# Performance work log

Hardware: AMD Instinct MI355X
Metric: run time of the kernel (lower is better)

Reference implementation:

```python
import jax, jax.numpy as jnp
import numpy as np

B, S, C, T = 256, 128, 64, 60
ENC, COL, RNN, ATT, ACT, TYP = 512, 512, 512, 512, 128, 64
NPROD, NTYPE = 97, 32
LS, PTEMP, CTEMP = 0.2, 1.0, 1.0
NEG = -1e9


def setup_inputs() -> dict:
    key = jax.random.key(0)
    ks = jax.random.split(key, 24)
    enc = jax.random.normal(ks[0], (B, S, ENC), jnp.float32)
    col_enc = jax.random.normal(ks[1], (B, C, COL), jnp.float32)
    enc_lens = jax.random.randint(ks[2], (B,), 1, S + 1)
    col_lens = jax.random.randint(ks[3], (B,), 1, C + 1)
    action_kind = jax.random.randint(ks[4], (B, T), 0, 3)  # 0=ApplyRule,1=Reduce,2=SelectColumn
    tgt_lens = jax.random.randint(ks[5], (B,), 1, T + 1)
    prod_ids = jax.random.randint(ks[6], (B, T), 0, NPROD)
    col_ids = jax.random.randint(ks[7], (B, T), 0, C) % col_lens[:, None]
    parent_prod = jax.random.randint(ks[8], (B, T), 0, NPROD)
    parent_type = jax.random.randint(ks[9], (B, T), 0, NTYPE)
    parent_time = jax.random.randint(ks[10], (B, T), 0, T) % jnp.maximum(jnp.arange(T), 1)[None, :]
    g = lambda k, shp: jax.random.normal(k, shp, jnp.float32) * 0.02
    IN = ACT + ATT + ACT + TYP + RNN  # a_tm1 | att_tm1 | parent_prod | parent_type | parent_h
    return dict(
        enc=enc, col_enc=col_enc, enc_lens=enc_lens, col_lens=col_lens,
        action_kind=action_kind, tgt_lens=tgt_lens, prod_ids=prod_ids,
        col_ids=col_ids, parent_prod=parent_prod, parent_type=parent_type,
        parent_time=parent_time,
        prod_embed=g(ks[11], (NPROD + 1, ACT)),
        type_embed=g(ks[12], (NTYPE, TYP)),
        b_lin=jnp.zeros((NPROD + 1,), jnp.float32),
        W_ih=g(ks[13], (IN, 4 * RNN)), W_hh=g(ks[14], (RNN, 4 * RNN)),
        b_lstm=jnp.zeros((4 * RNN,), jnp.float32),
        W_att_q=g(ks[15], (RNN, ENC)),
        W_att_vec=g(ks[16], (ENC + RNN, ATT)),
        W_r1=g(ks[17], (ATT, 4 * ATT)), b_r1=jnp.zeros((4 * ATT,), jnp.float32),
        W_r2=g(ks[18], (4 * ATT, ACT)), b_r2=jnp.zeros((ACT,), jnp.float32),
        W_col_in=g(ks[19], (COL, ACT)),
        W_ptr=g(ks[20], (ATT, COL)),
        w_mem=g(ks[21], (ATT, 1)),
    )


def reference(enc, col_enc, enc_lens, col_lens, action_kind, tgt_lens, prod_ids,
              col_ids, parent_prod, parent_type, parent_time,
              prod_embed, type_embed, b_lin, W_ih, W_hh, b_lstm,
              W_att_q, W_att_vec, W_r1, b_r1, W_r2, b_r2,
              W_col_in, W_ptr, w_mem):
    enc_mask = jnp.arange(S)[None, :] < enc_lens[:, None]   # [B,S]
    col_valid = jnp.arange(C)[None, :] < col_lens[:, None]  # [B,C]
    col_in_embed = jnp.einsum('bcd,da->bca', col_enc, W_col_in)  # column_rnn_input, [B,C,ACT]

    # previous-step actions (a_{t-1}); dummy zeros at t=0 (x is zeroed there anyway)
    shift = lambda a: jnp.concatenate([jnp.zeros_like(a[:, :1]), a[:, :-1]], axis=1)
    kind_p, pid_p, cid_p = shift(action_kind), shift(prod_ids), shift(col_ids)

    def scan_step(carry, xs):
        h, c, att, hist, appear, acc = carry
        t, kp, pp, cp, kind, pid, cid, fprod, ftype, ptime = xs
        # --- prep step input ---
        prev_valid = (t - 1) < tgt_lens
        e_rule = prod_embed[jnp.where(kp == 1, NPROD, pp)]                      # [B,ACT]
        e_col = jnp.take_along_axis(col_in_embed, cp[:, None, None], axis=1)[:, 0]
        a_embed = jnp.where((kp == 2)[:, None], e_col, e_rule)
        a_embed = jnp.where(prev_valid[:, None], a_embed, 0.0)
        parent_h = hist[ptime, jnp.arange(B)]                                   # [B,RNN]
        x = jnp.concatenate([a_embed, att, prod_embed[fprod], type_embed[ftype], parent_h], axis=-1)
        x = jnp.where(t == 0, 0.0, x)
        # --- LSTMCell (torch gate order i,f,g,o) ---
        gates = x @ W_ih + h @ W_hh + b_lstm
        i, f, g_, o = jnp.split(gates, 4, axis=-1)
        c_new = jax.nn.sigmoid(f) * c + jax.nn.sigmoid(i) * jnp.tanh(g_)
        h_new = jax.nn.sigmoid(o) * jnp.tanh(c_new)
        # --- attention over encoder ---
        scores = jnp.einsum('bd,bsd->bs', h_new @ W_att_q, enc)
        scores = jnp.where(enc_mask, scores, NEG)
        ctx = jnp.einsum('bs,bsd->bd', jax.nn.softmax(scores, axis=-1), enc)
        att_new = jnp.tanh(jnp.concatenate([ctx, h_new], axis=-1) @ W_att_vec)
        # --- production readout (tied output embedding) ---
        emb_q = jnp.tanh(att_new @ W_r1 + b_r1) @ W_r2 + b_r2
        rule_lp = jax.nn.log_softmax((emb_q @ prod_embed.T + b_lin) / PTEMP, axis=-1)
        # --- pointer net over columns with memory gate ---
        gate = jax.nn.sigmoid(att_new @ w_mem)                                  # [B,1]
        w_c = jnp.einsum('bd,bcd->bc', att_new @ W_ptr, col_enc)
        weights = w_c * appear * gate + w_c * (1.0 - appear) * (1.0 - gate)
        weights = jnp.where(col_valid, weights, NEG) / CTEMP
        col_lp = jax.nn.log_softmax(weights, axis=-1)
        # --- per-example log prob of gold action ---
        valid = t < tgt_lens
        lp_rule = jnp.take_along_axis(rule_lp, jnp.where(kind == 1, NPROD, pid)[:, None], axis=1)[:, 0]
        lp_col_raw = jnp.take_along_axis(col_lp, cid[:, None], axis=1)[:, 0]
        col_sum = jnp.sum(jnp.where(col_valid, col_lp, 0.0), axis=-1)
        lp_col = (1.0 - LS) * lp_col_raw + LS * col_sum / col_lens
        lp = jnp.where(kind == 2, lp_col, lp_rule)
        acc = acc + jnp.where(valid, lp, 0.0)
        # --- state updates (appear mask updated after use, matching torch) ---
        appear = jnp.maximum(appear, ((kind == 2) & valid)[:, None] * jax.nn.one_hot(cid, C, dtype=appear.dtype))
        hist = hist.at[t].set(h_new)
        return (h_new, c_new, att_new, hist, appear, acc), None

    carry0 = (
        jnp.zeros((B, RNN), jnp.float32), jnp.zeros((B, RNN), jnp.float32),
        jnp.zeros((B, ATT), jnp.float32), jnp.zeros((T, B, RNN), jnp.float32),
        jnp.zeros((B, C), jnp.float32), jnp.zeros((B,), jnp.float32),
    )
    xs = (jnp.arange(T), kind_p.T, pid_p.T, cid_p.T, action_kind.T, prod_ids.T,
          col_ids.T, parent_prod.T, parent_type.T, parent_time.T)
    (_, _, _, _, _, acc), _ = jax.lax.scan(scan_step, carry0, xs)
    return -jnp.mean(acc)
```

## Files before the change

### kernel.cpp

```cpp
#include <hip/hip_runtime.h>
#include <math.h>

#define NB 256
#define NS 128
#define NCOL 64
#define NT 60
#define DENC 512
#define DRNN 512
#define DATT 512
#define DACT 128
#define DTYP 64
#define DG 2048
#define NEGV (-1e9f)
#define NBH 131072
#define NROW 15360
#define RPW 512
#define NRP 2624

typedef unsigned short ushort_t;
typedef __attribute__((ext_vector_type(8))) short short8;
typedef __attribute__((ext_vector_type(4))) float f32x4;

__device__ __forceinline__ float sigf(float x) { return 1.0f / (1.0f + __expf(-x)); }
__device__ __forceinline__ float tanhfast(float x) {
  x = fminf(fmaxf(x, -15.0f), 15.0f);
  float e = __expf(-2.0f * x);
  return (1.0f - e) / (1.0f + e);
}
__device__ __forceinline__ ushort_t f2bf(float f) {
  union { float f; unsigned u; } v; v.f = f;
  unsigned r = v.u + 0x7fffu + ((v.u >> 16) & 1u);
  return (ushort_t)(r >> 16);
}
__device__ __forceinline__ float bf2f(ushort_t b) {
  union { unsigned u; float f; } v; v.u = ((unsigned)b) << 16; return v.f;
}
__device__ __forceinline__ short8 cvt8(const float* p) {
  f32x4 x = *(const f32x4*)p, y = *(const f32x4*)(p + 4);
  short8 r;
  r[0]=(short)f2bf(x[0]); r[1]=(short)f2bf(x[1]); r[2]=(short)f2bf(x[2]); r[3]=(short)f2bf(x[3]);
  r[4]=(short)f2bf(y[0]); r[5]=(short)f2bf(y[1]); r[6]=(short)f2bf(y[2]); r[7]=(short)f2bf(y[3]);
  return r;
}

__global__ __launch_bounds__(256) void zero_kernel(float* __restrict__ p, int n) {
  int i = blockIdx.x * 256 + threadIdx.x;
  if (i < n) p[i] = 0.0f;
}

__global__ __launch_bounds__(256) void cvt_bf16_kernel(const float* __restrict__ src,
    ushort_t* __restrict__ dst, int n8)
{
  int i = blockIdx.x * 256 + threadIdx.x;
  if (i < n8) *(short8*)&dst[(size_t)i * 8] = cvt8(src + (size_t)i * 8);
}

__global__ __launch_bounds__(256) void pack_w(const float* __restrict__ src,
    ushort_t* __restrict__ dst, int Ksub, int Nsub, int Ntot, int K0, int N0, int ldsrc)
{
  int idx = blockIdx.x * 256 + threadIdx.x;
  if (idx >= Ksub * Nsub) return;
  int k = idx / Nsub, n = idx - k * Nsub;
  int gk = K0 + k;
  dst[((size_t)(gk >> 3) * Ntot + (N0 + n)) * 8 + (gk & 7)] =
      f2bf(src[(size_t)k * ldsrc + n]);
}

__global__ __launch_bounds__(256) void pack_wT(const float* __restrict__ W,
    ushort_t* __restrict__ dst)
{
  int idx = blockIdx.x * 256 + threadIdx.x;
  if (idx >= 512 * 512) return;
  int r = idx >> 9, d = idx & 511;
  dst[((size_t)(d >> 3) * 512 + r) * 8 + (d & 7)] = f2bf(W[(size_t)r * 512 + d]);
}

__global__ __launch_bounds__(256) void r2p_kernel(const float* __restrict__ W_r2,
    const float* __restrict__ prod_embed, const float* __restrict__ b_r2,
    const float* __restrict__ b_lin, ushort_t* __restrict__ Wr2p,
    float* __restrict__ bias2)
{
  int idx = blockIdx.x * 256 + threadIdx.x;
  if (idx >= 2049 * 98) return;
  int k = idx / 98, j = idx - k * 98;
  const float* pe = prod_embed + (size_t)j * DACT;
  if (k < 2048) {
    const float* wr = W_r2 + (size_t)k * DACT;
    float a = 0.f;
    #pragma unroll 8
    for (int d = 0; d < DACT; ++d) a = fmaf(wr[d], pe[d], a);
    Wr2p[((size_t)(k >> 3) * 128 + j) * 8 + (k & 7)] = f2bf(a);
  } else {
    float a = b_lin[j];
    #pragma unroll 8
    for (int d = 0; d < DACT; ++d) a = fmaf(b_r2[d], pe[d], a);
    bias2[j] = a;
  }
}

__global__ __launch_bounds__(64) void appear_kernel(const int* __restrict__ action_kind,
    const int* __restrict__ tgt_lens, const int* __restrict__ col_ids,
    float* __restrict__ appear_all)
{
  int b = blockIdx.x, c = threadIdx.x;
  float ap = 0.f;
  int tl = tgt_lens[b];
  for (int t = 0; t < NT; ++t) {
    appear_all[((size_t)t * NB + b) * 64 + c] = ap;
    if (t < tl && action_kind[b * NT + t] == 2 && col_ids[b * NT + t] == c) ap = 1.f;
  }
}

__global__ __launch_bounds__(256) void gemm_bf16(
    const float* __restrict__ A1, int lda1,
    const ushort_t* __restrict__ Bp, ushort_t* __restrict__ Cb, int ldc,
    int N, int K)
{
  __shared__ short As[2][4096];
  __shared__ short Bs[2][4096];
  const int tid = threadIdx.x;
  const int lane = tid & 63, w = tid >> 6;
  const int wr = w >> 1, wc = w & 1;
  const int mBase = blockIdx.y * 64, nBase = blockIdx.x * 64;
  const int nt = K >> 6;
  f32x4 ra0[2], ra1[2];
  short8 rb[2];
  auto issue = [&](int kt) {
    #pragma unroll
    for (int s = 0; s < 2; ++s) {
      int slot = tid + s * 256;
      int kc = slot >> 6, m = slot & 63;
      int k0 = (kt << 6) + kc * 8;
      const float* p = A1 + (size_t)(mBase + m) * lda1 + k0;
      ra0[s] = *(const f32x4*)p;
      ra1[s] = *(const f32x4*)(p + 4);
      rb[s] = *(const short8*)(Bp + ((size_t)(k0 >> 3) * N + nBase + m) * 8);
    }
  };
  auto store = [&](int buf) {
    #pragma unroll
    for (int s = 0; s < 2; ++s) {
      int slot = tid + s * 256;
      short8 av;
      av[0]=(short)f2bf(ra0[s][0]); av[1]=(short)f2bf(ra0[s][1]);
      av[2]=(short)f2bf(ra0[s][2]); av[3]=(short)f2bf(ra0[s][3]);
      av[4]=(short)f2bf(ra1[s][0]); av[5]=(short)f2bf(ra1[s][1]);
      av[6]=(short)f2bf(ra1[s][2]); av[7]=(short)f2bf(ra1[s][3]);
      *(short8*)&As[buf][slot * 8] = av;
      *(short8*)&Bs[buf][slot * 8] = rb[s];
    }
  };
  f32x4 z4 = {0.f,0.f,0.f,0.f};
  f32x4 acc[2][2] = {{z4,z4},{z4,z4}};
  issue(0); store(0);
  __syncthreads();
  int cur = 0;
  for (int kt = 0; kt < nt; ++kt) {
    bool more = (kt + 1 < nt);
    if (more) issue(kt + 1);
    #pragma unroll
    for (int kk = 0; kk < 2; ++kk) {
      int ko = kk * 4 + (lane >> 4);
      short8 af[2], bfr[2];
      #pragma unroll
      for (int f = 0; f < 2; ++f) {
        int row = wr * 32 + f * 16 + (lane & 15);
        af[f] = *(const short8*)&As[cur][(ko * 64 + row) * 8];
        int col = wc * 32 + f * 16 + (lane & 15);
        bfr[f] = *(const short8*)&Bs[cur][(ko * 64 + col) * 8];
      }
      #pragma unroll
      for (int i = 0; i < 2; ++i)
        #pragma unroll
        for (int j = 0; j < 2; ++j)
          acc[i][j] = __builtin_amdgcn_mfma_f32_16x16x32_bf16(af[i], bfr[j], acc[i][j], 0, 0, 0);
    }
    if (more) store(cur ^ 1);
    __syncthreads();
    cur ^= 1;
  }
  #pragma unroll
  for (int i = 0; i < 2; ++i)
    #pragma unroll
    for (int j = 0; j < 2; ++j)
      #pragma unroll
      for (int r = 0; r < 4; ++r) {
        int row = mBase + wr * 32 + i * 16 + (lane >> 4) * 4 + r;
        int col = nBase + wc * 32 + j * 16 + (lane & 15);
        Cb[(size_t)row * ldc + col] = f2bf(acc[i][j][r]);
      }
}

__global__ __launch_bounds__(256) void gemm_encwq(
    const float* __restrict__ enc, const ushort_t* __restrict__ WqTp,
    ushort_t* __restrict__ encWq, ushort_t* __restrict__ enc_b)
{
  __shared__ short Asm[32768];
  const int tid = threadIdx.x;
  const int lane = tid & 63, w = tid >> 6;
  const int wr = w >> 1, wc = w & 1;
  const int mBase = blockIdx.x * 64;
  #pragma unroll
  for (int it = 0; it < 16; ++it) {
    int o = tid + it * 256;
    int row = o >> 6, c = o & 63;
    short8 v = cvt8(enc + (size_t)(mBase + row) * 512 + c * 8);
    *(short8*)&Asm[row * 512 + ((c ^ (row & 7)) * 8)] = v;
    *(short8*)(enc_b + (size_t)(mBase + row) * 512 + c * 8) = v;
  }
  __syncthreads();
  for (int nt = 0; nt < 8; ++nt) {
    f32x4 z4 = {0.f,0.f,0.f,0.f};
    f32x4 acc[2][2] = {{z4,z4},{z4,z4}};
    short8 bb[2][4];
    auto loadBf = [&](int kt, short8* dst) {
      #pragma unroll
      for (int kk = 0; kk < 2; ++kk)
        #pragma unroll
        for (int f = 0; f < 2; ++f) {
          int ko = kt * 8 + kk * 4 + (lane >> 4);
          int col = nt * 64 + wc * 32 + f * 16 + (lane & 15);
          dst[kk * 2 + f] = *(const short8*)(WqTp + ((size_t)ko * 512 + col) * 8);
        }
    };
    loadBf(0, bb[0]);
    loadBf(1, bb[1]);
    #pragma unroll
    for (int kt = 0; kt < 8; ++kt) {
      short8 cur[4];
      #pragma unroll
      for (int i = 0; i < 4; ++i) cur[i] = bb[kt & 1][i];
      if (kt + 2 < 8) loadBf(kt + 2, bb[kt & 1]);
      #pragma unroll
      for (int kk = 0; kk < 2; ++kk) {
        int ko = kt * 8 + kk * 4 + (lane >> 4);
        short8 af[2];
        #pragma unroll
        for (int f = 0; f < 2; ++f) {
          int row = wr * 32 + f * 16 + (lane & 15);
          af[f] = *(const short8*)&Asm[row * 512 + ((ko ^ (row & 7)) * 8)];
        }
        #pragma unroll
        for (int i = 0; i < 2; ++i)
          #pragma unroll
          for (int j = 0; j < 2; ++j)
            acc[i][j] = __builtin_amdgcn_mfma_f32_16x16x32_bf16(af[i], cur[kk * 2 + j], acc[i][j], 0, 0, 0);
      }
    }
    #pragma unroll
    for (int i = 0; i < 2; ++i)
      #pragma unroll
      for (int j = 0; j < 2; ++j)
        #pragma unroll
        for (int r = 0; r < 4; ++r) {
          int row = mBase + wr * 32 + i * 16 + (lane >> 4) * 4 + r;
          int col = nt * 64 + wc * 32 + j * 16 + (lane & 15);
          encWq[(size_t)row * 512 + col] = f2bf(acc[i][j][r]);
        }
  }
}

template <class FA, class FB, class FE>
__device__ __forceinline__ void gemm_core(char* smem, FA loadA, FB loadB,
    int ktBeg, int ktEnd, FE epi)
{
  short* As = (short*)smem;
  short* Bs = (short*)smem + 8192;
  const int tid = threadIdx.x;
  const int lane = tid & 63, w = tid >> 6;
  const int wr = w >> 1, wc = w & 1;
  f32x4 z4 = {0.f,0.f,0.f,0.f};
  f32x4 acc[2][2] = {{z4,z4},{z4,z4}};
  short8 pa[2], pb[2];
  auto issue = [&](int kt) {
    #pragma unroll
    for (int s = 0; s < 2; ++s) {
      int slot = tid + s * 256;
      int kc = slot >> 6;
      int k = (kt << 6) + (kc << 3);
      pa[s] = loadA(k);
      pb[s] = loadB(slot & 63, k);
    }
  };
  auto store = [&](int buf) {
    #pragma unroll
    for (int s = 0; s < 2; ++s) {
      int slot = tid + s * 256;
      *(short8*)&As[buf * 4096 + slot * 8] = pa[s];
      *(short8*)&Bs[buf * 4096 + slot * 8] = pb[s];
    }
  };
  issue(ktBeg); store(0);
  __syncthreads();
  int cur = 0;
  for (int kt = ktBeg; kt < ktEnd; ++kt) {
    bool more = (kt + 1 < ktEnd);
    if (more) issue(kt + 1);
    #pragma unroll
    for (int kk = 0; kk < 2; ++kk) {
      int ko = kk * 4 + (lane >> 4);
      short8 af[2], bfr[2];
      #pragma unroll
      for (int f = 0; f < 2; ++f) {
        int row = wr * 32 + f * 16 + (lane & 15);
        af[f] = *(const short8*)&As[cur * 4096 + (ko * 64 + row) * 8];
        int col = wc * 32 + f * 16 + (lane & 15);
        bfr[f] = *(const short8*)&Bs[cur * 4096 + (ko * 64 + col) * 8];
      }
      #pragma unroll
      for (int i = 0; i < 2; ++i)
        #pragma unroll
        for (int j = 0; j < 2; ++j)
          acc[i][j] = __builtin_amdgcn_mfma_f32_16x16x32_bf16(af[i], bfr[j], acc[i][j], 0, 0, 0);
    }
    if (more) store(cur ^ 1);
    __syncthreads();
    cur ^= 1;
  }
  #pragma unroll
  for (int i = 0; i < 2; ++i)
    #pragma unroll
    for (int j = 0; j < 2; ++j)
      #pragma unroll
      for (int r = 0; r < 4; ++r) {
        int rl = wr * 32 + i * 16 + (lane >> 4) * 4 + r;
        int cl = wc * 32 + j * 16 + (lane & 15);
        epi(rl, cl, acc[i][j][r]);
      }
}

__global__ __launch_bounds__(256) void k1_gates(
    const int* __restrict__ action_kind, const int* __restrict__ tgt_lens,
    const int* __restrict__ prod_ids, const int* __restrict__ col_ids,
    const int* __restrict__ parent_prod, const int* __restrict__ parent_type,
    const int* __restrict__ parent_time,
    const float* __restrict__ prod_embed, const float* __restrict__ type_embed,
    const ushort_t* __restrict__ WpG, const ushort_t* __restrict__ colin_b,
    const ushort_t* __restrict__ att_all, const ushort_t* __restrict__ hist_u,
    float* __restrict__ gates0, float* __restrict__ gates1,
    float* __restrict__ gates2, float* __restrict__ gates3, int t)
{
  __shared__ __align__(16) char smem[32768];
  const int tid = threadIdx.x;
  const int nb = blockIdx.x, mb = blockIdx.y, ks = blockIdx.z;
  const int mBase = mb * 64, nBase = nb * 64;
  const int b = mBase + (tid & 63);
  int kp = action_kind[b * NT + t - 1];
  int pp = prod_ids[b * NT + t - 1];
  int cp = col_ids[b * NT + t - 1];
  bool pv = (t - 1) < tgt_lens[b];
  int fp = parent_prod[b * NT + t];
  int ft = parent_type[b * NT + t];
  int ptm = parent_time[b * NT + t];
  const ushort_t* hist_prev = hist_u + (size_t)(t - 1) * NBH;
  const ushort_t* att_prev = att_all + (size_t)(t - 1) * NB * DATT;
  auto loadA = [&](int k) -> short8 {
    short8 z = {0,0,0,0,0,0,0,0};
    if (k < 128) {
      if (!pv) return z;
      if (kp == 2) return *(const short8*)(colin_b + ((size_t)(b * NCOL + cp) * DACT + k));
      int row = (kp == 1) ? 97 : pp;
      return cvt8(prod_embed + (size_t)row * DACT + k);
    } else if (k < 640) {
      return *(const short8*)(att_prev + (size_t)b * DATT + (k - 128));
    } else if (k < 768) {
      return cvt8(prod_embed + (size_t)fp * DACT + (k - 640));
    } else if (k < 832) {
      return cvt8(type_embed + (size_t)ft * DTYP + (k - 768));
    } else if (k < 1344) {
      return *(const short8*)(hist_u + (size_t)ptm * NBH + (size_t)b * DRNN + (k - 832));
    } else {
      return *(const short8*)(hist_prev + (size_t)b * DRNN + (k - 1344));
    }
  };
  auto loadB = [&](int n, int k) -> short8 {
    return *(const short8*)(WpG + ((size_t)(k >> 3) * DG + nBase + n) * 8);
  };
  float* gp = (ks == 0) ? gates0 : (ks == 1) ? gates1 : (ks == 2) ? gates2 : gates3;
  auto epi = [&](int rl, int cl, float v) {
    gp[(size_t)(mBase + rl) * DG + nBase + cl] = v;
  };
  const int kb0 = (ks == 0) ? 0 : (ks == 1) ? 8 : (ks == 2) ? 15 : 22;
  const int kb1 = (ks == 0) ? 8 : (ks == 1) ? 15 : (ks == 2) ? 22 : 29;
  gemm_core(smem, loadA, loadB, kb0, kb1, epi);
}

struct SmemK23 { float hq[DRNN]; float ml[4][2]; float cs[4][DENC]; };
__global__ __launch_bounds__(256) void k23_lstm_attn(
    const float* __restrict__ g0, const float* __restrict__ g1,
    const float* __restrict__ g2, const float* __restrict__ g3,
    const float* __restrict__ b_lstm, float* __restrict__ cst,
    ushort_t* __restrict__ hist_t,
    const ushort_t* __restrict__ encWq, const ushort_t* __restrict__ enc_b,
    const int* __restrict__ enc_lens, ushort_t* __restrict__ ctxb)
{
  __shared__ __align__(16) SmemK23 s;
  int b = blockIdx.x, tid = threadIdx.x;
  const float* p0 = g0 + (size_t)b * DG;
  const float* p1 = g1 + (size_t)b * DG;
  const float* p2 = g2 + (size_t)b * DG;
  const float* p3 = g3 + (size_t)b * DG;
  #pragma unroll
  for (int r = 0; r < 2; ++r) {
    int j = tid + r * 256;
    float gi = p0[j] + p1[j] + p2[j] + p3[j] + b_lstm[j];
    float gf = p0[512+j] + p1[512+j] + p2[512+j] + p3[512+j] + b_lstm[512+j];
    float gg = p0[1024+j] + p1[1024+j] + p2[1024+j] + p3[1024+j] + b_lstm[1024+j];
    float go = p0[1536+j] + p1[1536+j] + p2[1536+j] + p3[1536+j] + b_lstm[1536+j];
    size_t ix = (size_t)b * DRNN + j;
    float cn = sigf(gf) * cst[ix] + sigf(gi) * tanhfast(gg);
    float hn = sigf(go) * tanhfast(cn);
    cst[ix] = cn;
    hist_t[ix] = f2bf(hn);
    s.hq[j] = hn;
  }
  __syncthreads();
  int w = tid >> 6, lane = tid & 63;
  int el = enc_lens[b];
  float q[8];
  #pragma unroll
  for (int j = 0; j < 8; ++j) q[j] = s.hq[lane * 8 + j];
  float m = -1e30f, lr = 0.f;
  float cacc[8];
  #pragma unroll
  for (int j = 0; j < 8; ++j) cacc[j] = 0.f;
  const ushort_t* eWb = encWq + (size_t)b * NS * DENC + lane * 8;
  const ushort_t* eb = enc_b + (size_t)b * NS * DENC + lane * 8;
  for (int sI = w; sI < el; sI += 4) {
    short8 xr = *(const short8*)(eWb + (size_t)sI * DENC);
    short8 er = *(const short8*)(eb + (size_t)sI * DENC);
    float d = 0.f;
    #pragma unroll
    for (int j = 0; j < 8; ++j) d = fmaf(bf2f((ushort_t)xr[j]), q[j], d);
    #pragma unroll
    for (int off = 32; off > 0; off >>= 1) d += __shfl_xor(d, off);
    float mn = fmaxf(m, d);
    float rr = __expf(m - mn), p = __expf(d - mn);
    lr = lr * rr + p;
    #pragma unroll
    for (int j = 0; j < 8; ++j) cacc[j] = cacc[j] * rr + p * bf2f((ushort_t)er[j]);
    m = mn;
  }
  if (lane == 0) { s.ml[w][0] = m; s.ml[w][1] = lr; }
  #pragma unroll
  for (int j = 0; j < 8; ++j) s.cs[w][lane * 8 + j] = cacc[j];
  __syncthreads();
  float M = fmaxf(fmaxf(s.ml[0][0], s.ml[1][0]), fmaxf(s.ml[2][0], s.ml[3][0]));
  float f0 = __expf(s.ml[0][0] - M), f1 = __expf(s.ml[1][0] - M);
  float f2 = __expf(s.ml[2][0] - M), f3 = __expf(s.ml[3][0] - M);
  float invL = 1.f / (f0 * s.ml[0][1] + f1 * s.ml[1][1] + f2 * s.ml[2][1] + f3 * s.ml[3][1]);
  #pragma unroll
  for (int rep = 0; rep < 2; ++rep) {
    int d = tid + rep * 256;
    ctxb[(size_t)b * DENC + d] =
        f2bf((f0 * s.cs[0][d] + f1 * s.cs[1][d] + f2 * s.cs[2][d] + f3 * s.cs[3][d]) * invL);
  }
}

__global__ __launch_bounds__(256) void k4_attvec(const ushort_t* __restrict__ ctxb,
    const ushort_t* __restrict__ hist_t, const ushort_t* __restrict__ WpV,
    ushort_t* __restrict__ att_all, int t)
{
  __shared__ __align__(16) char smem[32768];
  const int tid = threadIdx.x;
  const int mBase = blockIdx.y * 64, nBase = blockIdx.x * 64;
  const int b = mBase + (tid & 63);
  auto loadA = [&](int k) -> short8 {
    if (k < 512) return *(const short8*)(ctxb + (size_t)b * DENC + k);
    return *(const short8*)(hist_t + (size_t)b * DRNN + (k - 512));
  };
  auto loadB = [&](int n, int k) -> short8 {
    return *(const short8*)(WpV + ((size_t)(k >> 3) * 512 + nBase + n) * 8);
  };
  auto epi = [&](int rl, int cl, float v) {
    att_all[((size_t)t * NB + mBase + rl) * DATT + nBase + cl] = f2bf(tanhfast(v));
  };
  gemm_core(smem, loadA, loadB, 0, 16, epi);
}

__global__ __launch_bounds__(256) void kbig_r1ptr(const ushort_t* __restrict__ att_all,
    const ushort_t* __restrict__ WpRP, const float* __restrict__ b_r1,
    ushort_t* __restrict__ r1c, ushort_t* __restrict__ ptrq_all,
    float* __restrict__ gate_all, int rowBase)
{
  __shared__ __align__(16) char smem[32768];
  const int tid = threadIdx.x;
  const int bid = blockIdx.x;
  const int x = bid & 7, j = bid >> 3;
  const int mb = x * 15 + j / 41;
  const int nb = j % 41;
  const int mBase = mb * 64, nBase = nb * 64;
  const size_t grow = (size_t)rowBase + mBase + (tid & 63);
  auto loadA = [&](int k) -> short8 {
    return *(const short8*)(att_all + grow * DATT + k);
  };
  auto loadB = [&](int n, int k) -> short8 {
    return *(const short8*)(WpRP + ((size_t)(k >> 3) * NRP + nBase + n) * 8);
  };
  auto epi = [&](int rl, int cl, float v) {
    int col = nBase + cl;
    size_t gr = (size_t)rowBase + mBase + rl;
    if (col < 2048)      r1c[(size_t)(mBase + rl) * DG + col] = f2bf(tanhfast(v + b_r1[col]));
    else if (col < 2560) ptrq_all[((size_t)(gr & 255) * NT + (gr >> 8)) * RPW + (col - 2048)] = f2bf(v);
    else if (col == 2560) gate_all[gr] = v;
  };
  gemm_core(smem, loadA, loadB, 0, 8, epi);
}

__global__ __launch_bounds__(256) void klogits(const ushort_t* __restrict__ r1c,
    const ushort_t* __restrict__ Wr2p, float* __restrict__ logits_all, int rowBase)
{
  __shared__ __align__(16) char smem[32768];
  const int tid = threadIdx.x;
  const int bid = blockIdx.x;
  const int x = bid & 7, j = bid >> 3;
  const int mb = x * 15 + (j >> 1);
  const int nb = j & 1;
  const int mBase = mb * 64, nBase = nb * 64;
  auto loadA = [&](int k) -> short8 {
    return *(const short8*)(r1c + (size_t)(mBase + (tid & 63)) * DG + k);
  };
  auto loadB = [&](int n, int k) -> short8 {
    return *(const short8*)(Wr2p + ((size_t)(k >> 3) * 128 + nBase + n) * 8);
  };
  auto epi = [&](int rl, int cl, float v) {
    logits_all[((size_t)rowBase + mBase + rl) * 128 + nBase + cl] = v;
  };
  gemm_core(smem, loadA, loadB, 0, 32, epi);
}

__global__ __launch_bounds__(256) void kwc(const ushort_t* __restrict__ ptrq_all,
    const ushort_t* __restrict__ colenc_b, float* __restrict__ w_c_all)
{
  __shared__ __align__(16) char smem[32768];
  const int tid = threadIdx.x;
  const int b = blockIdx.x;
  const int tt = tid & 63;
  auto loadA = [&](int k) -> short8 {
    short8 z = {0,0,0,0,0,0,0,0};
    if (tt >= NT) return z;
    return *(const short8*)(ptrq_all + ((size_t)b * NT + tt) * RPW + k);
  };
  auto loadB = [&](int n, int k) -> short8 {
    return *(const short8*)(colenc_b + ((size_t)b * NCOL + n) * 512 + k);
  };
  auto epi = [&](int rl, int cl, float v) {
    if (rl < NT) w_c_all[((size_t)rl * NB + b) * 64 + cl] = v;
  };
  gemm_core(smem, loadA, loadB, 0, 8, epi);
}

__global__ __launch_bounds__(64) void kfinal(
    const float* __restrict__ logits_all, const float* __restrict__ bias2,
    const float* __restrict__ w_c_all, const float* __restrict__ gate_all,
    const float* __restrict__ appear_all, const int* __restrict__ col_lens,
    const int* __restrict__ tgt_lens, const int* __restrict__ action_kind,
    const int* __restrict__ prod_ids, const int* __restrict__ col_ids,
    float* __restrict__ loss_tb)
{
  int row = blockIdx.x;
  int t = row >> 8, b = row & 255;
  int c = threadIdx.x;
  float l0 = logits_all[(size_t)row * 128 + c] + bias2[c];
  float l1 = (c + 64 < 98) ? logits_all[(size_t)row * 128 + 64 + c] + bias2[64 + c] : -1e30f;
  float m = fmaxf(l0, l1);
  #pragma unroll
  for (int off = 32; off > 0; off >>= 1) m = fmaxf(m, __shfl_down(m, off));
  m = __shfl(m, 0);
  float sv = __expf(l0 - m) + ((c + 64 < 98) ? __expf(l1 - m) : 0.f);
  #pragma unroll
  for (int off = 32; off > 0; off >>= 1) sv += __shfl_down(sv, off);
  sv = __shfl(sv, 0);
  float lseR = m + __logf(sv);
  int clen = col_lens[b];
  float gate = sigf(gate_all[row]);
  float ap = appear_all[(size_t)row * 64 + c];
  float wc = w_c_all[(size_t)row * 64 + c];
  float wv = wc * (ap * gate + (1.f - ap) * (1.f - gate));
  wv = (c < clen) ? wv : NEGV;
  float m2 = wv;
  #pragma unroll
  for (int off = 32; off > 0; off >>= 1) m2 = fmaxf(m2, __shfl_down(m2, off));
  m2 = __shfl(m2, 0);
  float s2 = __expf(wv - m2);
  #pragma unroll
  for (int off = 32; off > 0; off >>= 1) s2 += __shfl_down(s2, off);
  s2 = __shfl(s2, 0);
  float lse2 = m2 + __logf(s2);
  float csum = (c < clen) ? (wv - lse2) : 0.f;
  #pragma unroll
  for (int off = 32; off > 0; off >>= 1) csum += __shfl_down(csum, off);
  int kind = action_kind[b * NT + t];
  int cid = col_ids[b * NT + t];
  float wcid = __shfl(wv, cid);
  if (c == 0) {
    int pid = prod_ids[b * NT + t];
    bool valid = t < tgt_lens[b];
    int gj = (kind == 1) ? 97 : pid;
    float lgj = logits_all[(size_t)row * 128 + gj] + bias2[gj];
    float lp_rule = lgj - lseR;
    float lp_col = 0.8f * (wcid - lse2) + 0.2f * csum / (float)clen;
    float lp = (kind == 2) ? lp_col : lp_rule;
    loss_tb[row] = valid ? lp : 0.f;
  }
}

__global__ __launch_bounds__(256) void loss_reduce(const float* __restrict__ loss_tb,
                                                   float* __restrict__ out) {
  int tid = threadIdx.x;
  float v = 0.f;
  for (int k = 0; k < NT; ++k) v += loss_tb[(size_t)k * NB + tid];
  #pragma unroll
  for (int off = 32; off > 0; off >>= 1) v += __shfl_down(v, off);
  __shared__ float part[4];
  if ((tid & 63) == 0) part[tid >> 6] = v;
  __syncthreads();
  if (tid == 0) out[0] = -(part[0] + part[1] + part[2] + part[3]) * (1.0f / NB);
}

extern "C" void kernel_launch(void* const* d_in, const int* in_sizes, int n_in,
                              void* d_out, int out_size, void* d_ws, size_t ws_size,
                              hipStream_t stream) {
  const float* enc         = (const float*)d_in[0];
  const float* col_enc     = (const float*)d_in[1];
  const int*   enc_lens    = (const int*)d_in[2];
  const int*   col_lens    = (const int*)d_in[3];
  const int*   action_kind = (const int*)d_in[4];
  const int*   tgt_lens    = (const int*)d_in[5];
  const int*   prod_ids    = (const int*)d_in[6];
  const int*   col_ids     = (const int*)d_in[7];
  const int*   parent_prod = (const int*)d_in[8];
  const int*   parent_type = (const int*)d_in[9];
  const int*   parent_time = (const int*)d_in[10];
  const float* prod_embed  = (const float*)d_in[11];
  const float* type_embed  = (const float*)d_in[12];
  const float* b_lin       = (const float*)d_in[13];
  const float* W_ih        = (const float*)d_in[14];
  const float* W_hh        = (const float*)d_in[15];
  const float* b_lstm      = (const float*)d_in[16];
  const float* W_att_q     = (const float*)d_in[17];
  const float* W_att_vec   = (const float*)d_in[18];
  const float* W_r1        = (const float*)d_in[19];
  const float* b_r1        = (const float*)d_in[20];
  const float* W_r2        = (const float*)d_in[21];
  const float* b_r2        = (const float*)d_in[22];
  const float* W_col_in    = (const float*)d_in[23];
  const float* W_ptr       = (const float*)d_in[24];
  const float* w_mem       = (const float*)d_in[25];

  float* base = (float*)d_ws;
  size_t o = 0;
  float* cst    = base + o; o += 131072;
  float* gates0 = base + o; o += 524288;
  float* gates1 = base + o; o += 524288;
  float* gates2 = base + o; o += 524288;
  float* gates3 = base + o; o += 524288;
  int zeroN = (int)o;
  ushort_t* hist_u = (ushort_t*)(base + o); o += 3932160;
  float* logits_all = (float*)hist_u;
  ushort_t* colin_b = (ushort_t*)(base + o); o += 1048576;
  float* encWq_f    = base + o; o += 8388608;
  ushort_t* encWq   = (ushort_t*)encWq_f;
  ushort_t* r1c     = (ushort_t*)encWq_f;
  float* encb_f     = base + o; o += 4194304;
  ushort_t* enc_b   = (ushort_t*)encb_f;
  ushort_t* colenc_b = (ushort_t*)encb_f;
  ushort_t* att_all  = (ushort_t*)(base + o); o += 3932160;
  ushort_t* ptrq_all = (ushort_t*)(base + o); o += 3932160;
  ushort_t* ctxb     = ptrq_all;
  float* gate_all    = base + o; o += 15360;
  float* w_c_all     = base + o; o += 983040;
  float* appear_all  = base + o; o += 983040;
  float* loss_tb     = base + o; o += 15360;
  ushort_t* WpG   = (ushort_t*)(base + o); o += 1900544;
  ushort_t* WqTp  = (ushort_t*)(base + o); o += 131072;
  ushort_t* WpV   = (ushort_t*)(base + o); o += 262144;
  ushort_t* WpRP  = (ushort_t*)(base + o); o += 671744;
  ushort_t* WpCI  = (ushort_t*)(base + o); o += 32768;
  ushort_t* Wr2p  = (ushort_t*)(base + o); o += 131072;
  float* bias2    = base + o; o += 128;
  (void)ws_size; (void)in_sizes; (void)n_in; (void)out_size;

  zero_kernel<<<(zeroN + 255) / 256, 256, 0, stream>>>(base, zeroN);
  zero_kernel<<<(671744 + 255) / 256, 256, 0, stream>>>((float*)WpRP, 671744);
  zero_kernel<<<(131072 + 255) / 256, 256, 0, stream>>>((float*)Wr2p, 131072);

  pack_w<<<(1344 * 2048 + 255) / 256, 256, 0, stream>>>(W_ih, WpG, 1344, 2048, 2048, 0, 0, 2048);
  pack_w<<<(512 * 2048 + 255) / 256, 256, 0, stream>>>(W_hh, WpG, 512, 2048, 2048, 1344, 0, 2048);
  pack_wT<<<(512 * 512 + 255) / 256, 256, 0, stream>>>(W_att_q, WqTp);
  pack_w<<<(1024 * 512 + 255) / 256, 256, 0, stream>>>(W_att_vec, WpV, 1024, 512, 512, 0, 0, 512);
  pack_w<<<(512 * 2048 + 255) / 256, 256, 0, stream>>>(W_r1, WpRP, 512, 2048, NRP, 0, 0, 2048);
  pack_w<<<(512 * 512 + 255) / 256, 256, 0, stream>>>(W_ptr, WpRP, 512, 512, NRP, 0, 2048, 512);
  pack_w<<<(512 + 255) / 256, 256, 0, stream>>>(w_mem, WpRP, 512, 1, NRP, 0, 2560, 1);
  pack_w<<<(512 * 128 + 255) / 256, 256, 0, stream>>>(W_col_in, WpCI, 512, 128, 128, 0, 0, 128);
  r2p_kernel<<<(2049 * 98 + 255) / 256, 256, 0, stream>>>(W_r2, prod_embed, b_r2, b_lin, Wr2p, bias2);
  appear_kernel<<<NB, 64, 0, stream>>>(action_kind, tgt_lens, col_ids, appear_all);

  gemm_bf16<<<dim3(2, 256), 256, 0, stream>>>(col_enc, 512, WpCI, colin_b, 128, 128, 512);
  gemm_encwq<<<512, 256, 0, stream>>>(enc, WqTp, encWq, enc_b);

  for (int t = 0; t < NT; ++t) {
    ushort_t* hist_t = hist_u + (size_t)t * NBH;
    if (t > 0)
      k1_gates<<<dim3(32, 4, 4), 256, 0, stream>>>(
          action_kind, tgt_lens, prod_ids, col_ids, parent_prod, parent_type,
          parent_time, prod_embed, type_embed, WpG, colin_b, att_all, hist_u,
          gates0, gates1, gates2, gates3, t);
    k23_lstm_attn<<<NB, 256, 0, stream>>>(gates0, gates1, gates2, gates3,
        b_lstm, cst, hist_t, encWq, enc_b, enc_lens, ctxb);
    k4_attvec<<<dim3(8, 4), 256, 0, stream>>>(ctxb, hist_t, WpV, att_all, t);
  }

  cvt_bf16_kernel<<<(1048576 + 255) / 256, 256, 0, stream>>>(col_enc, colenc_b, 1048576);
  for (int ch = 0; ch < 2; ++ch) {
    int rowBase = ch * 7680;
    kbig_r1ptr<<<4920, 256, 0, stream>>>(att_all, WpRP, b_r1, r1c,
                                         ptrq_all, gate_all, rowBase);
    klogits<<<240, 256, 0, stream>>>(r1c, Wr2p, logits_all, rowBase);
  }
  kwc<<<NB, 256, 0, stream>>>(ptrq_all, colenc_b, w_c_all);
  kfinal<<<NROW, 64, 0, stream>>>(logits_all, bias2, w_c_all, gate_all,
      appear_all, col_lens, tgt_lens, action_kind, prod_ids, col_ids, loss_tb);
  loss_reduce<<<1, 256, 0, stream>>>(loss_tb, (float*)d_out);
}
```

Before: 3.072 ms.

## Split attention across two blocks per batch, bf16 gate partials, wider r1/ptr GEMM tiles

Gate partial sums from the split-K gate GEMM are now stored as bf16 instead of fp32, halving that traffic. The LSTM+attention kernel runs two blocks per batch row, each covering half the source positions, and writes unnormalized partial contexts plus max/sum so the att-vec GEMM merges them during its A-load. The post-loop r1/ptr GEMM switches to 64x128 tiles with register-prefetched double-buffered LDS and padded N. The changes trade some precision in the gates and duplicated LSTM cell math for more parallelism and less memory traffic.

Result: no change. 3.117 ms (+1.5%).

```diff
diff --git a/kernel.cpp b/kernel.cpp
--- a/kernel.cpp
+++ b/kernel.cpp
@@ -15,7 +15,7 @@
 #define NBH 131072
 #define NROW 15360
 #define RPW 512
-#define NRP 2624
+#define NRP 2688
 
 typedef unsigned short ushort_t;
 typedef __attribute__((ext_vector_type(8))) short short8;
@@ -337,8 +337,8 @@
     const float* __restrict__ prod_embed, const float* __restrict__ type_embed,
     const ushort_t* __restrict__ WpG, const ushort_t* __restrict__ colin_b,
     const ushort_t* __restrict__ att_all, const ushort_t* __restrict__ hist_u,
-    float* __restrict__ gates0, float* __restrict__ gates1,
-    float* __restrict__ gates2, float* __restrict__ gates3, int t)
+    ushort_t* __restrict__ gates0, ushort_t* __restrict__ gates1,
+    ushort_t* __restrict__ gates2, ushort_t* __restrict__ gates3, int t)
 {
   __shared__ __align__(16) char smem[32768];
   const int tid = threadIdx.x;
@@ -376,47 +376,59 @@
   auto loadB = [&](int n, int k) -> short8 {
     return *(const short8*)(WpG + ((size_t)(k >> 3) * DG + nBase + n) * 8);
   };
-  float* gp = (ks == 0) ? gates0 : (ks == 1) ? gates1 : (ks == 2) ? gates2 : gates3;
+  ushort_t* gp = (ks == 0) ? gates0 : (ks == 1) ? gates1 : (ks == 2) ? gates2 : gates3;
   auto epi = [&](int rl, int cl, float v) {
-    gp[(size_t)(mBase + rl) * DG + nBase + cl] = v;
+    gp[(size_t)(mBase + rl) * DG + nBase + cl] = f2bf(v);
   };
   const int kb0 = (ks == 0) ? 0 : (ks == 1) ? 8 : (ks == 2) ? 15 : 22;
   const int kb1 = (ks == 0) ? 8 : (ks == 1) ? 15 : (ks == 2) ? 22 : 29;
   gemm_core(smem, loadA, loadB, kb0, kb1, epi);
 }
 
-struct SmemK23 { float hq[DRNN]; float ml[4][2]; float cs[4][DENC]; };
+struct SmemK23 { float g4[2048]; float hq[DRNN]; float ml[4][2]; float cs[4][DENC]; };
 __global__ __launch_bounds__(256) void k23_lstm_attn(
-    const float* __restrict__ g0, const float* __restrict__ g1,
-    const float* __restrict__ g2, const float* __restrict__ g3,
+    const ushort_t* __restrict__ g0, const ushort_t* __restrict__ g1,
+    const ushort_t* __restrict__ g2, const ushort_t* __restrict__ g3,
     const float* __restrict__ b_lstm, float* __restrict__ cst,
     ushort_t* __restrict__ hist_t,
     const ushort_t* __restrict__ encWq, const ushort_t* __restrict__ enc_b,
-    const int* __restrict__ enc_lens, ushort_t* __restrict__ ctxb)
+    const int* __restrict__ enc_lens, float* __restrict__ ctxP,
+    float* __restrict__ mlP)
 {
   __shared__ __align__(16) SmemK23 s;
-  int b = blockIdx.x, tid = threadIdx.x;
-  const float* p0 = g0 + (size_t)b * DG;
-  const float* p1 = g1 + (size_t)b * DG;
-  const float* p2 = g2 + (size_t)b * DG;
-  const float* p3 = g3 + (size_t)b * DG;
+  int bid = blockIdx.x, tid = threadIdx.x;
+  int b = bid >> 1, half = bid & 1;
+  {
+    int sec = tid >> 6;
+    int jj = (tid & 63) * 8;
+    size_t off = (size_t)b * DG + sec * 512 + jj;
+    short8 v0 = *(const short8*)(g0 + off);
+    short8 v1 = *(const short8*)(g1 + off);
+    short8 v2 = *(const short8*)(g2 + off);
+    short8 v3 = *(const short8*)(g3 + off);
+    #pragma unroll
+    for (int e = 0; e < 8; ++e)
+      s.g4[sec * 512 + jj + e] = bf2f((ushort_t)v0[e]) + bf2f((ushort_t)v1[e])
+          + bf2f((ushort_t)v2[e]) + bf2f((ushort_t)v3[e]) + b_lstm[sec * 512 + jj + e];
+  }
+  __syncthreads();
   #pragma unroll
   for (int r = 0; r < 2; ++r) {
     int j = tid + r * 256;
-    float gi = p0[j] + p1[j] + p2[j] + p3[j] + b_lstm[j];
-    float gf = p0[512+j] + p1[512+j] + p2[512+j] + p3[512+j] + b_lstm[512+j];
-    float gg = p0[1024+j] + p1[1024+j] + p2[1024+j] + p3[1024+j] + b_lstm[1024+j];
-    float go = p0[1536+j] + p1[1536+j] + p2[1536+j] + p3[1536+j] + b_lstm[1536+j];
+    float gi = s.g4[j], gf = s.g4[512 + j], gg = s.g4[1024 + j], go = s.g4[1536 + j];
     size_t ix = (size_t)b * DRNN + j;
     float cn = sigf(gf) * cst[ix] + sigf(gi) * tanhfast(gg);
     float hn = sigf(go) * tanhfast(cn);
-    cst[ix] = cn;
-    hist_t[ix] = f2bf(hn);
+    if (half == 0) {
+      cst[ix] = cn;
+      hist_t[ix] = f2bf(hn);
+    }
     s.hq[j] = hn;
   }
   __syncthreads();
   int w = tid >> 6, lane = tid & 63;
   int el = enc_lens[b];
+  int hi = min(el, half * 64 + 64);
   float q[8];
   #pragma unroll
   for (int j = 0; j < 8; ++j) q[j] = s.hq[lane * 8 + j];
@@ -426,7 +438,7 @@
   for (int j = 0; j < 8; ++j) cacc[j] = 0.f;
   const ushort_t* eWb = encWq + (size_t)b * NS * DENC + lane * 8;
   const ushort_t* eb = enc_b + (size_t)b * NS * DENC + lane * 8;
-  for (int sI = w; sI < el; sI += 4) {
+  for (int sI = half * 64 + w; sI < hi; sI += 4) {
     short8 xr = *(const short8*)(eWb + (size_t)sI * DENC);
     short8 er = *(const short8*)(eb + (size_t)sI * DENC);
     float d = 0.f;
@@ -448,25 +460,43 @@
   float M = fmaxf(fmaxf(s.ml[0][0], s.ml[1][0]), fmaxf(s.ml[2][0], s.ml[3][0]));
   float f0 = __expf(s.ml[0][0] - M), f1 = __expf(s.ml[1][0] - M);
   float f2 = __expf(s.ml[2][0] - M), f3 = __expf(s.ml[3][0] - M);
-  float invL = 1.f / (f0 * s.ml[0][1] + f1 * s.ml[1][1] + f2 * s.ml[2][1] + f3 * s.ml[3][1]);
+  float L = f0 * s.ml[0][1] + f1 * s.ml[1][1] + f2 * s.ml[2][1] + f3 * s.ml[3][1];
   #pragma unroll
   for (int rep = 0; rep < 2; ++rep) {
     int d = tid + rep * 256;
-    ctxb[(size_t)b * DENC + d] =
-        f2bf((f0 * s.cs[0][d] + f1 * s.cs[1][d] + f2 * s.cs[2][d] + f3 * s.cs[3][d]) * invL);
-  }
-}
-
-__global__ __launch_bounds__(256) void k4_attvec(const ushort_t* __restrict__ ctxb,
-    const ushort_t* __restrict__ hist_t, const ushort_t* __restrict__ WpV,
-    ushort_t* __restrict__ att_all, int t)
+    ctxP[(size_t)bid * DENC + d] =
+        f0 * s.cs[0][d] + f1 * s.cs[1][d] + f2 * s.cs[2][d] + f3 * s.cs[3][d];
+  }
+  if (tid == 0) { mlP[bid * 2] = M; mlP[bid * 2 + 1] = L; }
+}
+
+__global__ __launch_bounds__(256) void k4_attvec(const float* __restrict__ ctxP,
+    const float* __restrict__ mlP, const ushort_t* __restrict__ hist_t,
+    const ushort_t* __restrict__ WpV, ushort_t* __restrict__ att_all, int t)
 {
   __shared__ __align__(16) char smem[32768];
   const int tid = threadIdx.x;
   const int mBase = blockIdx.y * 64, nBase = blockIdx.x * 64;
   const int b = mBase + (tid & 63);
+  float m0 = mlP[(b * 2) * 2],     l0 = mlP[(b * 2) * 2 + 1];
+  float m1 = mlP[(b * 2 + 1) * 2], l1 = mlP[(b * 2 + 1) * 2 + 1];
+  float M = fmaxf(m0, m1);
+  float f0 = __expf(m0 - M), f1 = __expf(m1 - M);
+  float invL = 1.f / (f0 * l0 + f1 * l1);
+  const float* c0 = ctxP + (size_t)(b * 2) * DENC;
+  const float* c1 = ctxP + (size_t)(b * 2 + 1) * DENC;
   auto loadA = [&](int k) -> short8 {
-    if (k < 512) return *(const short8*)(ctxb + (size_t)b * DENC + k);
+    if (k < 512) {
+      f32x4 a0 = *(const f32x4*)(c0 + k), a1 = *(const f32x4*)(c0 + k + 4);
+      f32x4 b0 = *(const f32x4*)(c1 + k), b1 = *(const f32x4*)(c1 + k + 4);
+      short8 r;
+      #pragma unroll
+      for (int e = 0; e < 4; ++e) {
+        r[e]     = (short)f2bf((f0 * a0[e] + f1 * b0[e]) * invL);
+        r[e + 4] = (short)f2bf((f0 * a1[e] + f1 * b1[e]) * invL);
+      }
+      return r;
+    }
     return *(const short8*)(hist_t + (size_t)b * DRNN + (k - 512));
   };
   auto loadB = [&](int n, int k) -> short8 {
@@ -483,28 +513,92 @@
     ushort_t* __restrict__ r1c, ushort_t* __restrict__ ptrq_all,
     float* __restrict__ gate_all, int rowBase)
 {
-  __shared__ __align__(16) char smem[32768];
+  __shared__ short As[2][4096];
+  __shared__ short Bs[2][8192];
   const int tid = threadIdx.x;
+  const int lane = tid & 63, w = tid >> 6;
+  const int wr = w >> 1, wc = w & 1;
   const int bid = blockIdx.x;
   const int x = bid & 7, j = bid >> 3;
-  const int mb = x * 15 + j / 41;
-  const int nb = j % 41;
-  const int mBase = mb * 64, nBase = nb * 64;
-  const size_t grow = (size_t)rowBase + mBase + (tid & 63);
-  auto loadA = [&](int k) -> short8 {
-    return *(const short8*)(att_all + grow * DATT + k);
-  };
-  auto loadB = [&](int n, int k) -> short8 {
-    return *(const short8*)(WpRP + ((size_t)(k >> 3) * NRP + nBase + n) * 8);
-  };
-  auto epi = [&](int rl, int cl, float v) {
-    int col = nBase + cl;
-    size_t gr = (size_t)rowBase + mBase + rl;
-    if (col < 2048)      r1c[(size_t)(mBase + rl) * DG + col] = f2bf(tanhfast(v + b_r1[col]));
-    else if (col < 2560) ptrq_all[((size_t)(gr & 255) * NT + (gr >> 8)) * RPW + (col - 2048)] = f2bf(v);
-    else if (col == 2560) gate_all[gr] = v;
-  };
-  gemm_core(smem, loadA, loadB, 0, 8, epi);
+  const int mb = x * 15 + j / 21;
+  const int ng = j % 21;
+  const int mBase = mb * 64, nBase = ng * 128;
+  const size_t grow = (size_t)rowBase + mBase + lane;
+  short8 pa[2], pb[4];
+  auto issue = [&](int kt) {
+    #pragma unroll
+    for (int s = 0; s < 2; ++s) {
+      int slot = tid + s * 256;
+      int kc = slot >> 6, m = slot & 63;
+      int k = (kt << 6) + (kc << 3);
+      pa[s] = *(const short8*)(att_all + ((size_t)rowBase + mBase + m) * DATT + k);
+    }
+    #pragma unroll
+    for (int s = 0; s < 4; ++s) {
+      int slot = tid + s * 256;
+      int kc = slot >> 7, n = slot & 127;
+      int k = (kt << 6) + (kc << 3);
+      pb[s] = *(const short8*)(WpRP + ((size_t)(k >> 3) * NRP + nBase + n) * 8);
+    }
+  };
+  auto store = [&](int buf) {
+    #pragma unroll
+    for (int s = 0; s < 2; ++s) {
+      int slot = tid + s * 256;
+      *(short8*)&As[buf][slot * 8] = pa[s];
+    }
+    #pragma unroll
+    for (int s = 0; s < 4; ++s) {
+      int slot = tid + s * 256;
+      *(short8*)&Bs[buf][slot * 8] = pb[s];
+    }
+  };
+  f32x4 z4 = {0.f,0.f,0.f,0.f};
+  f32x4 acc[2][4] = {{z4,z4,z4,z4},{z4,z4,z4,z4}};
+  issue(0); store(0);
+  __syncthreads();
+  int cur = 0;
+  for (int kt = 0; kt < 8; ++kt) {
+    bool more = (kt + 1 < 8);
+    if (more) issue(kt + 1);
+    #pragma unroll
+    for (int kk = 0; kk < 2; ++kk) {
+      int ko = kk * 4 + (lane >> 4);
+      short8 af[2], bfr[4];
+      #pragma unroll
+      for (int f = 0; f < 2; ++f) {
+        int row = wr * 32 + f * 16 + (lane & 15);
+        af[f] = *(const short8*)&As[cur][(ko * 64 + row) * 8];
+      }
+      #pragma unroll
+      for (int f = 0; f < 4; ++f) {
+        int col = wc * 64 + f * 16 + (lane & 15);
+        bfr[f] = *(const short8*)&Bs[cur][(ko * 128 + col) * 8];
+      }
+      #pragma unroll
+      for (int i = 0; i < 2; ++i)
+        #pragma unroll
+        for (int jf = 0; jf < 4; ++jf)
+          acc[i][jf] = __builtin_amdgcn_mfma_f32_16x16x32_bf16(af[i], bfr[jf], acc[i][jf], 0, 0, 0);
+    }
+    if (more) store(cur ^ 1);
+    __syncthreads();
+    cur ^= 1;
+  }
+  #pragma unroll
+  for (int i = 0; i < 2; ++i)
+    #pragma unroll
+    for (int jf = 0; jf < 4; ++jf)
+      #pragma unroll
+      for (int r = 0; r < 4; ++r) {
+        int rl = wr * 32 + i * 16 + (lane >> 4) * 4 + r;
+        int col = nBase + wc * 64 + jf * 16 + (lane & 15);
+        size_t gr = (size_t)rowBase + mBase + rl;
+        float v = acc[i][jf][r];
+        if (col < 2048)      r1c[(size_t)(mBase + rl) * DG + col] = f2bf(tanhfast(v + b_r1[col]));
+        else if (col < 2560) ptrq_all[((size_t)(gr & 255) * NT + (gr >> 8)) * RPW + (col - 2048)] = f2bf(v);
+        else if (col == 2560) gate_all[gr] = v;
+      }
 }
 
 __global__ __launch_bounds__(256) void klogits(const ushort_t* __restrict__ r1c,
@@ -651,10 +745,10 @@
   float* base = (float*)d_ws;
   size_t o = 0;
   float* cst    = base + o; o += 131072;
-  float* gates0 = base + o; o += 524288;
-  float* gates1 = base + o; o += 524288;
-  float* gates2 = base + o; o += 524288;
-  float* gates3 = base + o; o += 524288;
+  ushort_t* gates0 = (ushort_t*)(base + o); o += 262144;
+  ushort_t* gates1 = (ushort_t*)(base + o); o += 262144;
+  ushort_t* gates2 = (ushort_t*)(base + o); o += 262144;
+  ushort_t* gates3 = (ushort_t*)(base + o); o += 262144;
   int zeroN = (int)o;
   ushort_t* hist_u = (ushort_t*)(base + o); o += 3932160;
   float* logits_all = (float*)hist_u;
@@ -667,7 +761,8 @@
   ushort_t* colenc_b = (ushort_t*)encb_f;
   ushort_t* att_all  = (ushort_t*)(base + o); o += 3932160;
   ushort_t* ptrq_all = (ushort_t*)(base + o); o += 3932160;
-  ushort_t* ctxb     = ptrq_all;
+  float* ctxP        = (float*)ptrq_all;
+  float* mlP         = ctxP + 262144;
   float* gate_all    = base + o; o += 15360;
   float* w_c_all     = base + o; o += 983040;
   float* appear_all  = base + o; o += 983040;
@@ -675,14 +770,14 @@
   ushort_t* WpG   = (ushort_t*)(base + o); o += 1900544;
   ushort_t* WqTp  = (ushort_t*)(base + o); o += 131072;
   ushort_t* WpV   = (ushort_t*)(base + o); o += 262144;
-  ushort_t* WpRP  = (ushort_t*)(base + o); o += 671744;
+  ushort_t* WpRP  = (ushort_t*)(base + o); o += 688128;
   ushort_t* WpCI  = (ushort_t*)(base + o); o += 32768;
   ushort_t* Wr2p  = (ushort_t*)(base + o); o += 131072;
   float* bias2    = base + o; o += 128;
   (void)ws_size; (void)in_sizes; (void)n_in; (void)out_size;
 
   zero_kernel<<<(zeroN + 255) / 256, 256, 0, stream>>>(base, zeroN);
-  zero_kernel<<<(671744 + 255) / 256, 256, 0, stream>>>((float*)WpRP, 671744);
+  zero_kernel<<<(688128 + 255) / 256, 256, 0, stream>>>((float*)WpRP, 688128);
   zero_kernel<<<(131072 + 255) / 256, 256, 0, stream>>>((float*)Wr2p, 131072);
 
   pack_w<<<(1344 * 2048 + 255) / 256, 256, 0, stream>>>(W_ih, WpG, 1344, 2048, 2048, 0, 0, 2048);
@@ -706,15 +801,15 @@
           action_kind, tgt_lens, prod_ids, col_ids, parent_prod, parent_type,
           parent_time, prod_embed, type_embed, WpG, colin_b, att_all, hist_u,
           gates0, gates1, gates2, gates3, t);
-    k23_lstm_attn<<<NB, 256, 0, stream>>>(gates0, gates1, gates2, gates3,
-        b_lstm, cst, hist_t, encWq, enc_b, enc_lens, ctxb);
-    k4_attvec<<<dim3(8, 4), 256, 0, stream>>>(ctxb, hist_t, WpV, att_all, t);
+    k23_lstm_attn<<<NB * 2, 256, 0, stream>>>(gates0, gates1, gates2, gates3,
+        b_lstm, cst, hist_t, encWq, enc_b, enc_lens, ctxP, mlP);
+    k4_attvec<<<dim3(8, 4), 256, 0, stream>>>(ctxP, mlP, hist_t, WpV, att_all, t);
   }
 
   cvt_bf16_kernel<<<(1048576 + 255) / 256, 256, 0, stream>>>(col_enc, colenc_b, 1048576);
   for (int ch = 0; ch < 2; ++ch) {
     int rowBase = ch * 7680;
-    kbig_r1ptr<<<4920, 256, 0, stream>>>(att_all, WpRP, b_r1, r1c,
+    kbig_r1ptr<<<2520, 256, 0, stream>>>(att_all, WpRP, b_r1, r1c,
                                          ptrq_all, gate_all, rowBase);
     klogits<<<240, 256, 0, stream>>>(r1c, Wr2p, logits_all, rowBase);
   }
```
